# Performance work log

Hardware: AMD Instinct MI355X
Metric: run time of the kernel (lower is better)

The kernel has to match this reference:

```python
import jax, jax.numpy as jnp
import numpy as np
from jax import lax
import math

D_MODEL, D_STATE, D_CONV, D_INNER, DT_RANK = 1024, 16, 4, 2048, 64
BATCH, SEQLEN = 2, 2048


def setup_inputs() -> dict:
    key = jax.random.key(0)
    ks = jax.random.split(key, 10)
    s = 0.02
    x = jax.random.normal(ks[0], (BATCH, SEQLEN, D_MODEL), jnp.float32)
    W_in = jax.random.normal(ks[1], (D_MODEL, 2 * D_INNER), jnp.float32) * s
    conv_w = jax.random.normal(ks[2], (D_INNER, 1, D_CONV), jnp.float32) * 0.2
    conv_b = jnp.zeros((D_INNER,), jnp.float32)
    W_x = jax.random.normal(ks[3], (D_INNER, DT_RANK + 2 * D_STATE), jnp.float32) * s
    W_dt = jax.random.normal(ks[4], (DT_RANK, D_INNER), jnp.float32) * s
    # dt bias init as in the torch module: inverse-softplus of dt ~ logU(1e-3, 1e-1)
    u = jax.random.uniform(ks[5], (D_INNER,), jnp.float32)
    dt = jnp.clip(jnp.exp(u * (math.log(0.1) - math.log(0.001)) + math.log(0.001)), 1e-4)
    b_dt = dt + jnp.log(-jnp.expm1(-dt))
    A_log = jnp.log(jnp.tile(jnp.arange(1, D_STATE + 1, dtype=jnp.float32)[None, :], (D_INNER, 1)))
    D = jnp.ones((D_INNER,), jnp.float32)
    W_out = jax.random.normal(ks[6], (D_INNER, D_MODEL), jnp.float32) * s
    return {"x": x, "W_in": W_in, "conv_w": conv_w, "conv_b": conv_b, "W_x": W_x,
            "W_dt": W_dt, "b_dt": b_dt, "A_log": A_log, "D": D, "W_out": W_out}


def _forward(x, W_in, conv_w, conv_b, W_x, W_dt, b_dt, A_log, D, W_out):
    b, l, _ = x.shape
    d_inner, d_state = A_log.shape
    d_conv = conv_w.shape[-1]
    dt_rank = W_dt.shape[0]

    xz = x @ W_in                                  # (b, l, 2*d_inner)
    xi, z = jnp.split(xz, 2, axis=-1)

    # depthwise causal conv1d (torch pads both sides by d_conv-1 then slices [:l])
    xc = jnp.transpose(xi, (0, 2, 1))              # (b, d_inner, l)
    xc = lax.conv_general_dilated(
        xc, conv_w, window_strides=(1,), padding=[(d_conv - 1, 0)],
        feature_group_count=d_inner,
        dimension_numbers=("NCH", "OIH", "NCH"))
    xc = xc + conv_b[None, :, None]
    xi = jax.nn.silu(jnp.transpose(xc, (0, 2, 1)))  # (b, l, d_inner)

    x_dbl = xi @ W_x                                # (b, l, dt_rank + 2*d_state)
    dt, B, C = jnp.split(x_dbl, [dt_rank, dt_rank + d_state], axis=-1)
    dt = jax.nn.softplus(dt @ W_dt + b_dt)          # (b, l, d_inner)
    A = -jnp.exp(A_log)                             # (d_inner, d_state)

    def step(h, inp):
        dt_t, B_t, C_t, x_t = inp                   # (b,d),(b,n),(b,n),(b,d)
        dA = jnp.exp(dt_t[..., None] * A)           # (b, d, n)
        dB = dt_t[..., None] * B_t[:, None, :]      # (b, d, n)
        h = dA * h + dB * x_t[..., None]
        y = jnp.einsum("bdn,bn->bd", h, C_t) + D * x_t
        return h, y

    xs = (jnp.transpose(dt, (1, 0, 2)), jnp.transpose(B, (1, 0, 2)),
          jnp.transpose(C, (1, 0, 2)), jnp.transpose(xi, (1, 0, 2)))
    h0 = jnp.zeros((b, d_inner, d_state), x.dtype)
    _, ys = lax.scan(step, h0, xs)                  # ys: (l, b, d_inner)
    y = jnp.transpose(ys, (1, 0, 2))

    y = y * jax.nn.silu(z)
    return y @ W_out                                # (b, l, d_model)


def reference(x, W_in, conv_w, conv_b, W_x, W_dt, b_dt, A_log, D, W_out):
    return _forward(x, W_in, conv_w, conv_b, W_x, W_dt, b_dt, A_log, D, W_out)
```

## Files before the change

### kernel.cpp

```cpp
#include <hip/hip_runtime.h>
#include <math.h>


#define D_INNER 2048
#define D_STATE 16
#define SEQLEN  2048
#define NBATCH  2
#define NCHUNK  32
#define CHUNKLEN (SEQLEN / NCHUNK)

using f32x4 = __attribute__((ext_vector_type(4))) float;
using s16x8 = __attribute__((ext_vector_type(8))) short;

__device__ __forceinline__ float siluf(float x) {
  return x / (1.f + __expf(-x));
}
__device__ __forceinline__ float softplusf(float x) {
  return fmaxf(x, 0.f) + log1pf(__expf(-fabsf(x)));
}

__device__ __forceinline__ void split_pair(float f0, float f1,
                                           unsigned& hw, unsigned& lw) {
  unsigned b0 = __float_as_uint(f0), b1 = __float_as_uint(f1);
  hw = (b0 >> 16) | (b1 & 0xFFFF0000u);
  float r0 = f0 - __uint_as_float(b0 & 0xFFFF0000u);
  float r1 = f1 - __uint_as_float(b1 & 0xFFFF0000u);
  unsigned c0 = __float_as_uint(r0); c0 += 0x7FFFu + ((c0 >> 16) & 1u);
  unsigned c1 = __float_as_uint(r1); c1 += 0x7FFFu + ((c1 >> 16) & 1u);
  lw = (c0 >> 16) | (c1 & 0xFFFF0000u);
}

__global__ __launch_bounds__(256) void packsplit_k(
    const float* __restrict__ in, unsigned* __restrict__ out)
{
  size_t g = (size_t)blockIdx.x * 256 + threadIdx.x;
  float f[32];
#pragma unroll
  for (int q = 0; q < 8; ++q)
    *(float4*)&f[q * 4] = *(const float4*)(in + g * 32 + q * 4);
  unsigned* o = out + g * 32;
#pragma unroll
  for (int j = 0; j < 16; ++j) {
    unsigned hw, lw;
    split_pair(f[2 * j], f[2 * j + 1], hw, lw);
    o[j] = hw; o[16 + j] = lw;
  }
}

__global__ __launch_bounds__(256) void packsplit_dt_k(
    const float* __restrict__ xdbl, unsigned* __restrict__ out)
{
  int g = blockIdx.x * 256 + threadIdx.x;
  int row = g >> 1, kc = g & 1;
  float f[32];
#pragma unroll
  for (int q = 0; q < 8; ++q)
    *(float4*)&f[q * 4] =
        *(const float4*)(xdbl + (size_t)row * 96 + kc * 32 + q * 4);
  unsigned* o = out + (size_t)g * 32;
#pragma unroll
  for (int j = 0; j < 16; ++j) {
    unsigned hw, lw;
    split_pair(f[2 * j], f[2 * j + 1], hw, lw);
    o[j] = hw; o[16 + j] = lw;
  }
}

__global__ __launch_bounds__(256) void transpack_k(
    const float* __restrict__ in, unsigned* __restrict__ out, int K, int N)
{
  __shared__ float tile[32][257];
  const int tid = threadIdx.x;
  const int nb = blockIdx.x * 256;
  const int kc = blockIdx.y;
#pragma unroll 8
  for (int ky = 0; ky < 32; ++ky)
    tile[ky][tid] = in[(size_t)(kc * 32 + ky) * N + nb + tid];
  __syncthreads();
  unsigned* o = out + ((size_t)(nb + tid) * (K >> 5) + kc) * 32;
#pragma unroll
  for (int j = 0; j < 16; ++j) {
    unsigned hw, lw;
    split_pair(tile[2 * j][tid], tile[2 * j + 1][tid], hw, lw);
    o[j] = hw; o[16 + j] = lw;
  }
}

__global__ __launch_bounds__(128) void transpack_wx_k(
    const float* __restrict__ Wx, unsigned* __restrict__ out)
{
  const int n = threadIdx.x;
  const int kc = blockIdx.x;
  float f[32];
#pragma unroll
  for (int j = 0; j < 32; ++j)
    f[j] = (n < 96) ? Wx[(size_t)(kc * 32 + j) * 96 + n] : 0.f;
  unsigned* o = out + ((size_t)n * 64 + kc) * 32;
#pragma unroll
  for (int j = 0; j < 16; ++j) {
    unsigned hw, lw;
    split_pair(f[2 * j], f[2 * j + 1], hw, lw);
    o[j] = hw; o[16 + j] = lw;
  }
}

template <int EPI>
__global__ __launch_bounds__(256, 2) void mgemm_split(
    const unsigned short* __restrict__ A, const unsigned short* __restrict__ Bt,
    const float* __restrict__ bias, float* __restrict__ C,
    int M, int N, int K, int ldc)
{
  __shared__ s16x8 AsV[128 * 8];
  __shared__ s16x8 BsV[128 * 8];

  const int tid = threadIdx.x;
  const int wv  = tid >> 6;
  const int ln  = tid & 63;
  const int wr  = wv >> 1, wc = wv & 1;
  const int m0  = blockIdx.y * 128, n0 = blockIdx.x * 128;
  const int K32 = K >> 5;

  const int rr = ln & 15;
  const int ko = ln >> 4;
  const int sh = ko ^ (rr & 7);
  const int sl = (4 | ko) ^ (rr & 7);
  const int srow  = ln >> 3;
  const int sslot = (ln & 7) ^ srow;

  f32x4 acc[4][4];
#pragma unroll
  for (int i = 0; i < 4; i++)
#pragma unroll
    for (int j = 0; j < 4; j++) acc[i][j] = (f32x4)0.f;

  for (int ktc = 0; ktc < K32; ++ktc) {
    __syncthreads();
#pragma unroll
    for (int t = 0; t < 4; ++t) {
      int i = wv * 4 + t;
      const unsigned short* ga =
          A + ((size_t)(m0 + i * 8 + srow) * K32 + ktc) * 64 + sslot * 8;
      const unsigned short* gb =
          Bt + ((size_t)(n0 + i * 8 + srow) * K32 + ktc) * 64 + sslot * 8;
      __builtin_amdgcn_global_load_lds(
          (const __attribute__((address_space(1))) void*)ga,
          (__attribute__((address_space(3))) void*)((char*)AsV + i * 1024), 16, 0, 0);
      __builtin_amdgcn_global_load_lds(
          (const __attribute__((address_space(1))) void*)gb,
          (__attribute__((address_space(3))) void*)((char*)BsV + i * 1024), 16, 0, 0);
    }
    __syncthreads();

    s16x8 ah[4], al[4], bh[4], bl[4];
#pragma unroll
    for (int mi = 0; mi < 4; ++mi) {
      int r = wr * 64 + mi * 16 + rr;
      ah[mi] = AsV[r * 8 + sh];
      al[mi] = AsV[r * 8 + sl];
    }
#pragma unroll
    for (int ni = 0; ni < 4; ++ni) {
      int c = wc * 64 + ni * 16 + rr;
      bh[ni] = BsV[c * 8 + sh];
      bl[ni] = BsV[c * 8 + sl];
    }
#pragma unroll
    for (int mi = 0; mi < 4; ++mi)
#pragma unroll
      for (int ni = 0; ni < 4; ++ni) {
        acc[mi][ni] = __builtin_amdgcn_mfma_f32_16x16x32_bf16(ah[mi], bh[ni], acc[mi][ni], 0, 0, 0);
        acc[mi][ni] = __builtin_amdgcn_mfma_f32_16x16x32_bf16(ah[mi], bl[ni], acc[mi][ni], 0, 0, 0);
        acc[mi][ni] = __builtin_amdgcn_mfma_f32_16x16x32_bf16(al[mi], bh[ni], acc[mi][ni], 0, 0, 0);
      }
  }

  const int orow = (ln >> 4) * 4;
#pragma unroll
  for (int mi = 0; mi < 4; ++mi)
#pragma unroll
    for (int ni = 0; ni < 4; ++ni) {
      int rowg = m0 + wr * 64 + mi * 16 + orow;
      int colg = n0 + wc * 64 + ni * 16 + rr;
      float bcol = (EPI == 1) ? bias[colg] : 0.f;
#pragma unroll
      for (int i = 0; i < 4; ++i) {
        float v = acc[mi][ni][i];
        if (EPI == 1) v = softplusf(v + bcol);
        C[(size_t)(rowg + i) * ldc + colg] = v;
      }
    }
}

__global__ __launch_bounds__(256, 2) void xdbl_mfma_k(
    const unsigned short* __restrict__ A, const unsigned short* __restrict__ Bt,
    float* __restrict__ P)
{
  __shared__ s16x8 AsV[128 * 8];
  __shared__ s16x8 BsV[128 * 8];

  const int tid = threadIdx.x;
  const int wv  = tid >> 6;
  const int ln  = tid & 63;
  const int wr  = wv >> 1, wc = wv & 1;
  const int kz  = blockIdx.x;
  const int m0  = blockIdx.y * 128;
  const int K32 = 64;

  const int rr = ln & 15;
  const int ko = ln >> 4;
  const int sh = ko ^ (rr & 7);
  const int sl = (4 | ko) ^ (rr & 7);
  const int srow  = ln >> 3;
  const int sslot = (ln & 7) ^ srow;

  f32x4 acc[4][4];
#pragma unroll
  for (int i = 0; i < 4; i++)
#pragma unroll
    for (int j = 0; j < 4; j++) acc[i][j] = (f32x4)0.f;

  for (int ktc = kz * 8; ktc < kz * 8 + 8; ++ktc) {
    __syncthreads();
#pragma unroll
    for (int t = 0; t < 4; ++t) {
      int i = wv * 4 + t;
      const unsigned short* ga =
          A + ((size_t)(m0 + i * 8 + srow) * K32 + ktc) * 64 + sslot * 8;
      const unsigned short* gb =
          Bt + ((size_t)(i * 8 + srow) * K32 + ktc) * 64 + sslot * 8;
      __builtin_amdgcn_global_load_lds(
          (const __attribute__((address_space(1))) void*)ga,
          (__attribute__((address_space(3))) void*)((char*)AsV + i * 1024), 16, 0, 0);
      __builtin_amdgcn_global_load_lds(
          (const __attribute__((address_space(1))) void*)gb,
          (__attribute__((address_space(3))) void*)((char*)BsV + i * 1024), 16, 0, 0);
    }
    __syncthreads();

    s16x8 ah[4], al[4], bh[4], bl[4];
#pragma unroll
    for (int mi = 0; mi < 4; ++mi) {
      int r = wr * 64 + mi * 16 + rr;
      ah[mi] = AsV[r * 8 + sh];
      al[mi] = AsV[r * 8 + sl];
    }
#pragma unroll
    for (int ni = 0; ni < 4; ++ni) {
      int c = wc * 64 + ni * 16 + rr;
      bh[ni] = BsV[c * 8 + sh];
      bl[ni] = BsV[c * 8 + sl];
    }
#pragma unroll
    for (int mi = 0; mi < 4; ++mi)
#pragma unroll
      for (int ni = 0; ni < 4; ++ni) {
        acc[mi][ni] = __builtin_amdgcn_mfma_f32_16x16x32_bf16(ah[mi], bh[ni], acc[mi][ni], 0, 0, 0);
        acc[mi][ni] = __builtin_amdgcn_mfma_f32_16x16x32_bf16(ah[mi], bl[ni], acc[mi][ni], 0, 0, 0);
        acc[mi][ni] = __builtin_amdgcn_mfma_f32_16x16x32_bf16(al[mi], bh[ni], acc[mi][ni], 0, 0, 0);
      }
  }

  const int orow = (ln >> 4) * 4;
#pragma unroll
  for (int mi = 0; mi < 4; ++mi)
#pragma unroll
    for (int ni = 0; ni < 4; ++ni) {
      int rowg = m0 + wr * 64 + mi * 16 + orow;
      int colg = wc * 64 + ni * 16 + rr;
      if (colg < 96) {
#pragma unroll
        for (int i = 0; i < 4; ++i)
          P[((size_t)kz * 4096 + rowg + i) * 96 + colg] = acc[mi][ni][i];
      }
    }
}

__global__ __launch_bounds__(256) void xdbl_reduce_k(
    const float* __restrict__ P, float* __restrict__ xdbl)
{
  int i = blockIdx.x * 256 + threadIdx.x;
  float s = 0.f;
#pragma unroll
  for (int kz = 0; kz < 8; ++kz) s += P[(size_t)kz * 393216 + i];
  xdbl[i] = s;
}

__global__ __launch_bounds__(256) void conv_silu_k(
    const float* __restrict__ xz, const float* __restrict__ cw,
    const float* __restrict__ cb, float* __restrict__ xi)
{
  int idx = blockIdx.x * 256 + threadIdx.x;
  int d = idx & (D_INNER - 1);
  int row = idx >> 11;
  int l = row & (SEQLEN - 1);
  float4 w = *(const float4*)(cw + d * 4);
  const float wv[4] = {w.x, w.y, w.z, w.w};
  float acc = cb[d];
#pragma unroll
  for (int j = 0; j < 4; j++) {
    int ll = l - 3 + j;
    if (ll >= 0)
      acc = fmaf(wv[j], xz[(size_t)(row - 3 + j) * 4096 + d], acc);
  }
  xi[idx] = siluf(acc);
}

__global__ __launch_bounds__(256) void aprep_k(const float* __restrict__ A_log,
                                               float* __restrict__ A2)
{
  int i = blockIdx.x * 256 + threadIdx.x;
  A2[i] = -__expf(A_log[i]);
}

__global__ __launch_bounds__(256) void scan_pass1(
    const float* __restrict__ dt, const float* __restrict__ xi,
    const float* __restrict__ xdbl, const float* __restrict__ A2,
    float* __restrict__ cP, float* __restrict__ cH)
{
  int d = blockIdx.x * 256 + threadIdx.x;
  int c = blockIdx.y;
  int b = blockIdx.z;
  float a2[D_STATE], h[D_STATE], P[D_STATE];
#pragma unroll
  for (int n = 0; n < D_STATE; n++) {
    a2[n] = A2[d * D_STATE + n];
    h[n] = 0.f;
    P[n] = 1.f;
  }
  int rowbase = b * SEQLEN + c * CHUNKLEN;
  for (int l = 0; l < CHUNKLEN; l++) {
    int row = rowbase + l;
    float dtv = dt[(size_t)row * D_INNER + d];
    float xv = xi[(size_t)row * D_INNER + d];
    float dtx = dtv * xv;
    const float* Bp = xdbl + (size_t)row * 96 + 64;
#pragma unroll
    for (int n = 0; n < D_STATE; n++) {
      float dA = __expf(dtv * a2[n]);
      P[n] *= dA;
      h[n] = fmaf(dA, h[n], dtx * Bp[n]);
    }
  }
  size_t base = ((size_t)(b * D_INNER + d) * NCHUNK + c) * D_STATE;
#pragma unroll
  for (int n = 0; n < D_STATE; n++) {
    cP[base + n] = P[n];
    cH[base + n] = h[n];
  }
}

__global__ __launch_bounds__(256) void scan_pass2(
    const float* __restrict__ cP, float* __restrict__ cH)
{
  int t = blockIdx.x * 256 + threadIdx.x;
  size_t base = (size_t)(t >> 4) * (NCHUNK * D_STATE) + (t & 15);
  float h = 0.f;
  for (int c = 0; c < NCHUNK; c++) {
    size_t idx = base + (size_t)c * D_STATE;
    float Pv = cP[idx];
    float q = cH[idx];
    cH[idx] = h;
    h = fmaf(Pv, h, q);
  }
}

__global__ __launch_bounds__(256) void scan_pass3(
    float* __restrict__ dtyg, const float* __restrict__ xi,
    const float* __restrict__ xdbl, const float* __restrict__ A2,
    const float* __restrict__ cH, const float* __restrict__ Dvec,
    const float* __restrict__ xz)
{
  int d = blockIdx.x * 256 + threadIdx.x;
  int c = blockIdx.y;
  int b = blockIdx.z;
  float a2[D_STATE], h[D_STATE];
  size_t base = ((size_t)(b * D_INNER + d) * NCHUNK + c) * D_STATE;
#pragma unroll
  for (int n = 0; n < D_STATE; n++) {
    a2[n] = A2[d * D_STATE + n];
    h[n] = cH[base + n];
  }
  float Dd = Dvec[d];
  int rowbase = b * SEQLEN + c * CHUNKLEN;
  for (int l = 0; l < CHUNKLEN; l++) {
    int row = rowbase + l;
    float dtv = dtyg[(size_t)row * D_INNER + d];
    float xv = xi[(size_t)row * D_INNER + d];
    float dtx = dtv * xv;
    const float* Bp = xdbl + (size_t)row * 96 + 64;
    const float* Cp = Bp + D_STATE;
    float y = Dd * xv;
#pragma unroll
    for (int n = 0; n < D_STATE; n++) {
      float dA = __expf(dtv * a2[n]);
      h[n] = fmaf(dA, h[n], dtx * Bp[n]);
      y = fmaf(h[n], Cp[n], y);
    }
    float z = xz[(size_t)row * 4096 + D_INNER + d];
    dtyg[(size_t)row * D_INNER + d] = y * siluf(z);
  }
}

extern "C" void kernel_launch(void* const* d_in, const int* in_sizes, int n_in,
                              void* d_out, int out_size, void* d_ws,
                              size_t ws_size, hipStream_t stream)
{
  const float* x     = (const float*)d_in[0];
  const float* W_in  = (const float*)d_in[1];
  const float* cw    = (const float*)d_in[2];
  const float* cb    = (const float*)d_in[3];
  const float* W_x   = (const float*)d_in[4];
  const float* W_dt  = (const float*)d_in[5];
  const float* b_dt  = (const float*)d_in[6];
  const float* A_log = (const float*)d_in[7];
  const float* Dv    = (const float*)d_in[8];
  const float* W_out = (const float*)d_in[9];
  float* out = (float*)d_out;

  float* ws    = (float*)d_ws;
  float* xz    = ws;
  float* xi    = xz + 16777216;
  float* xdbl  = xi + 8388608;
  float* dtyg  = xdbl + 393216;
  float* A2    = dtyg + 8388608;
  float* cP    = A2 + 32768;
  float* cH    = cP + 2097152;

  unsigned* WinTP  = (unsigned*)dtyg;
  unsigned* xP     = (unsigned*)(dtyg + 4194304);
  unsigned* xiP    = (unsigned*)dtyg;
  unsigned* WxTP   = (unsigned*)xdbl;
  float*    Ppart  = cP;
  unsigned* xdblP  = (unsigned*)cP;
  unsigned* WdtTP  = (unsigned*)cP + 262144;
  unsigned* ygP    = (unsigned*)xi;
  unsigned* WoutTP = (unsigned*)cP;

  aprep_k<<<128, 256, 0, stream>>>(A_log, A2);

  transpack_k<<<dim3(16, 32), 256, 0, stream>>>(W_in, WinTP, 1024, 4096);
  packsplit_k<<<512, 256, 0, stream>>>(x, xP);

  mgemm_split<0><<<dim3(32, 32), 256, 0, stream>>>(
      (const unsigned short*)xP, (const unsigned short*)WinTP, nullptr, xz,
      4096, 4096, 1024, 4096);

  conv_silu_k<<<32768, 256, 0, stream>>>(xz, cw, cb, xi);

  packsplit_k<<<1024, 256, 0, stream>>>(xi, xiP);
  transpack_wx_k<<<64, 128, 0, stream>>>(W_x, WxTP);
  xdbl_mfma_k<<<dim3(8, 32), 256, 0, stream>>>(
      (const unsigned short*)xiP, (const unsigned short*)WxTP, Ppart);
  xdbl_reduce_k<<<1536, 256, 0, stream>>>(Ppart, xdbl);

  packsplit_dt_k<<<32, 256, 0, stream>>>(xdbl, xdblP);
  transpack_k<<<dim3(8, 2), 256, 0, stream>>>(W_dt, WdtTP, 64, 2048);
  mgemm_split<1><<<dim3(16, 32), 256, 0, stream>>>(
      (const unsigned short*)xdblP, (const unsigned short*)WdtTP, b_dt, dtyg,
      4096, 2048, 64, 2048);

  scan_pass1<<<dim3(8, NCHUNK, NBATCH), 256, 0, stream>>>(dtyg, xi, xdbl, A2, cP, cH);
  scan_pass2<<<256, 256, 0, stream>>>(cP, cH);
  scan_pass3<<<dim3(8, NCHUNK, NBATCH), 256, 0, stream>>>(dtyg, xi, xdbl, A2, cH, Dv, xz);

  packsplit_k<<<1024, 256, 0, stream>>>(dtyg, ygP);
  transpack_k<<<dim3(4, 64), 256, 0, stream>>>(W_out, WoutTP, 2048, 1024);

  mgemm_split<0><<<dim3(8, 32), 256, 0, stream>>>(
      (const unsigned short*)ygP, (const unsigned short*)WoutTP, nullptr, out,
      4096, 1024, 2048, 1024);
}
```

Baseline: 486.6 us.

## Fuse hi/lo bf16 split packing into producer kernels and drop A prep kernel

```diff
diff --git a/kernel.cpp b/kernel.cpp
--- a/kernel.cpp
+++ b/kernel.cpp
@@ -30,6 +30,16 @@
   lw = (c0 >> 16) | (c1 & 0xFFFF0000u);
 }
 
+__device__ __forceinline__ void split_one(float v, unsigned short& hv,
+                                          unsigned short& lv) {
+  unsigned b = __float_as_uint(v);
+  hv = (unsigned short)(b >> 16);
+  float r = v - __uint_as_float(b & 0xFFFF0000u);
+  unsigned c = __float_as_uint(r);
+  c += 0x7FFFu + ((c >> 16) & 1u);
+  lv = (unsigned short)(c >> 16);
+}
+
 __global__ __launch_bounds__(256) void packsplit_k(
     const float* __restrict__ in, unsigned* __restrict__ out)
 {
@@ -39,25 +49,6 @@
   for (int q = 0; q < 8; ++q)
     *(float4*)&f[q * 4] = *(const float4*)(in + g * 32 + q * 4);
   unsigned* o = out + g * 32;
-#pragma unroll
-  for (int j = 0; j < 16; ++j) {
-    unsigned hw, lw;
-    split_pair(f[2 * j], f[2 * j + 1], hw, lw);
-    o[j] = hw; o[16 + j] = lw;
-  }
-}
-
-__global__ __launch_bounds__(256) void packsplit_dt_k(
-    const float* __restrict__ xdbl, unsigned* __restrict__ out)
-{
-  int g = blockIdx.x * 256 + threadIdx.x;
-  int row = g >> 1, kc = g & 1;
-  float f[32];
-#pragma unroll
-  for (int q = 0; q < 8; ++q)
-    *(float4*)&f[q * 4] =
-        *(const float4*)(xdbl + (size_t)row * 96 + kc * 32 + q * 4);
-  unsigned* o = out + (size_t)g * 32;
 #pragma unroll
   for (int j = 0; j < 16; ++j) {
     unsigned hw, lw;
@@ -108,7 +99,7 @@
 __global__ __launch_bounds__(256, 2) void mgemm_split(
     const unsigned short* __restrict__ A, const unsigned short* __restrict__ Bt,
     const float* __restrict__ bias, float* __restrict__ C,
-    int M, int N, int K, int ldc)
+    int M, int N, int K, int ldaC, int ldc)
 {
   __shared__ s16x8 AsV[128 * 8];
   __shared__ s16x8 BsV[128 * 8];
@@ -139,7 +130,7 @@
     for (int t = 0; t < 4; ++t) {
       int i = wv * 4 + t;
       const unsigned short* ga =
-          A + ((size_t)(m0 + i * 8 + srow) * K32 + ktc) * 64 + sslot * 8;
+          A + ((size_t)(m0 + i * 8 + srow) * ldaC + ktc) * 64 + sslot * 8;
       const unsigned short* gb =
           Bt + ((size_t)(n0 + i * 8 + srow) * K32 + ktc) * 64 + sslot * 8;
       __builtin_amdgcn_global_load_lds(
@@ -275,19 +266,31 @@
     }
 }
 
-__global__ __launch_bounds__(256) void xdbl_reduce_k(
-    const float* __restrict__ P, float* __restrict__ xdbl)
+__global__ __launch_bounds__(256) void xdbl_fuse_k(
+    const float* __restrict__ P, float* __restrict__ xdbl,
+    unsigned short* __restrict__ xdblPs)
 {
   int i = blockIdx.x * 256 + threadIdx.x;
   float s = 0.f;
 #pragma unroll
   for (int kz = 0; kz < 8; ++kz) s += P[(size_t)kz * 393216 + i];
-  xdbl[i] = s;
-}
-
-__global__ __launch_bounds__(256) void conv_silu_k(
+  int row = i / 96;
+  int col = i - row * 96;
+  if (col < 64) {
+    unsigned short hv, lv;
+    split_one(s, hv, lv);
+    size_t cb = ((size_t)row * 2 + (col >> 5)) * 64 + (col & 31);
+    xdblPs[cb] = hv;
+    xdblPs[cb + 32] = lv;
+  } else {
+    xdbl[i] = s;
+  }
+}
+
+__global__ __launch_bounds__(256) void conv_silu_pack_k(
     const float* __restrict__ xz, const float* __restrict__ cw,
-    const float* __restrict__ cb, float* __restrict__ xi)
+    const float* __restrict__ cb, float* __restrict__ xi,
+    unsigned short* __restrict__ xiPs)
 {
   int idx = blockIdx.x * 256 + threadIdx.x;
   int d = idx & (D_INNER - 1);
@@ -302,19 +305,18 @@
     if (ll >= 0)
       acc = fmaf(wv[j], xz[(size_t)(row - 3 + j) * 4096 + d], acc);
   }
-  xi[idx] = siluf(acc);
-}
-
-__global__ __launch_bounds__(256) void aprep_k(const float* __restrict__ A_log,
-                                               float* __restrict__ A2)
-{
-  int i = blockIdx.x * 256 + threadIdx.x;
-  A2[i] = -__expf(A_log[i]);
+  float v = siluf(acc);
+  xi[idx] = v;
+  unsigned short hv, lv;
+  split_one(v, hv, lv);
+  size_t cbase = ((size_t)row * 64 + (d >> 5)) * 64 + (d & 31);
+  xiPs[cbase] = hv;
+  xiPs[cbase + 32] = lv;
 }
 
 __global__ __launch_bounds__(256) void scan_pass1(
     const float* __restrict__ dt, const float* __restrict__ xi,
-    const float* __restrict__ xdbl, const float* __restrict__ A2,
+    const float* __restrict__ xdbl, const float* __restrict__ A_log,
     float* __restrict__ cP, float* __restrict__ cH)
 {
   int d = blockIdx.x * 256 + threadIdx.x;
@@ -323,7 +325,7 @@
   float a2[D_STATE], h[D_STATE], P[D_STATE];
 #pragma unroll
   for (int n = 0; n < D_STATE; n++) {
-    a2[n] = A2[d * D_STATE + n];
+    a2[n] = -__expf(A_log[d * D_STATE + n]);
     h[n] = 0.f;
     P[n] = 1.f;
   }
@@ -365,10 +367,10 @@
 }
 
 __global__ __launch_bounds__(256) void scan_pass3(
-    float* __restrict__ dtyg, const float* __restrict__ xi,
-    const float* __restrict__ xdbl, const float* __restrict__ A2,
+    const float* __restrict__ dt, const float* __restrict__ xi,
+    const float* __restrict__ xdbl, const float* __restrict__ A_log,
     const float* __restrict__ cH, const float* __restrict__ Dvec,
-    const float* __restrict__ xz)
+    float* __restrict__ xz)
 {
   int d = blockIdx.x * 256 + threadIdx.x;
   int c = blockIdx.y;
@@ -377,14 +379,15 @@
   size_t base = ((size_t)(b * D_INNER + d) * NCHUNK + c) * D_STATE;
 #pragma unroll
   for (int n = 0; n < D_STATE; n++) {
-    a2[n] = A2[d * D_STATE + n];
+    a2[n] = -__expf(A_log[d * D_STATE + n]);
     h[n] = cH[base + n];
   }
   float Dd = Dvec[d];
+  unsigned short* ygPs = (unsigned short*)xz;
   int rowbase = b * SEQLEN + c * CHUNKLEN;
   for (int l = 0; l < CHUNKLEN; l++) {
     int row = rowbase + l;
-    float dtv = dtyg[(size_t)row * D_INNER + d];
+    float dtv = dt[(size_t)row * D_INNER + d];
     float xv = xi[(size_t)row * D_INNER + d];
     float dtx = dtv * xv;
     const float* Bp = xdbl + (size_t)row * 96 + 64;
@@ -397,7 +400,12 @@
       y = fmaf(h[n], Cp[n], y);
     }
     float z = xz[(size_t)row * 4096 + D_INNER + d];
-    dtyg[(size_t)row * D_INNER + d] = y * siluf(z);
+    float g = y * siluf(z);
+    unsigned short hv, lv;
+    split_one(g, hv, lv);
+    size_t cb = (size_t)row * 8192 + (size_t)(d >> 5) * 64 + (d & 31);
+    ygPs[cb] = hv;
+    ygPs[cb + 32] = lv;
   }
 }
 
@@ -425,48 +433,44 @@
   float* A2    = dtyg + 8388608;
   float* cP    = A2 + 32768;
   float* cH    = cP + 2097152;
+  (void)A2;
 
   unsigned* WinTP  = (unsigned*)dtyg;
   unsigned* xP     = (unsigned*)(dtyg + 4194304);
   unsigned* xiP    = (unsigned*)dtyg;
   unsigned* WxTP   = (unsigned*)xdbl;
   float*    Ppart  = cP;
-  unsigned* xdblP  = (unsigned*)cP;
-  unsigned* WdtTP  = (unsigned*)cP + 262144;
-  unsigned* ygP    = (unsigned*)xi;
+  unsigned short* xdblPs = (unsigned short*)(cP + 3145728);
+  unsigned* WdtTP  = (unsigned*)(cP + 3145728 + 262144);
+  unsigned short* ygPs   = (unsigned short*)xz;
   unsigned* WoutTP = (unsigned*)cP;
-
-  aprep_k<<<128, 256, 0, stream>>>(A_log, A2);
 
   transpack_k<<<dim3(16, 32), 256, 0, stream>>>(W_in, WinTP, 1024, 4096);
   packsplit_k<<<512, 256, 0, stream>>>(x, xP);
 
   mgemm_split<0><<<dim3(32, 32), 256, 0, stream>>>(
       (const unsigned short*)xP, (const unsigned short*)WinTP, nullptr, xz,
-      4096, 4096, 1024, 4096);
-
-  conv_silu_k<<<32768, 256, 0, stream>>>(xz, cw, cb, xi);
-
-  packsplit_k<<<1024, 256, 0, stream>>>(xi, xiP);
+      4096, 4096, 1024, 32, 4096);
+
+  conv_silu_pack_k<<<32768, 256, 0, stream>>>(xz, cw, cb, xi, (unsigned short*)xiP);
+
   transpack_wx_k<<<64, 128, 0, stream>>>(W_x, WxTP);
   xdbl_mfma_k<<<dim3(8, 32), 256, 0, stream>>>(
       (const unsigned short*)xiP, (const unsigned short*)WxTP, Ppart);
-  xdbl_reduce_k<<<1536, 256, 0, stream>>>(Ppart, xdbl);
-
-  packsplit_dt_k<<<32, 256, 0, stream>>>(xdbl, xdblP);
+  xdbl_fuse_k<<<1536, 256, 0, stream>>>(Ppart, xdbl, xdblPs);
+
   transpack_k<<<dim3(8, 2), 256, 0, stream>>>(W_dt, WdtTP, 64, 2048);
   mgemm_split<1><<<dim3(16, 32), 256, 0, stream>>>(
-      (const unsigned short*)xdblP, (const unsigned short*)WdtTP, b_dt, dtyg,
-      4096, 2048, 64, 2048);
-
-  scan_pass1<<<dim3(8, NCHUNK, NBATCH), 256, 0, stream>>>(dtyg, xi, xdbl, A2, cP, cH);
+      xdblPs, (const unsigned short*)WdtTP, b_dt, dtyg,
+      4096, 2048, 64, 2, 2048);
+
+  scan_pass1<<<dim3(8, NCHUNK, NBATCH), 256, 0, stream>>>(dtyg, xi, xdbl, A_log, cP, cH);
   scan_pass2<<<256, 256, 0, stream>>>(cP, cH);
-  scan_pass3<<<dim3(8, NCHUNK, NBATCH), 256, 0, stream>>>(dtyg, xi, xdbl, A2, cH, Dv, xz);
-
-  packsplit_k<<<1024, 256, 0, stream>>>(dtyg, ygP);
+  scan_pass3<<<dim3(8, NCHUNK, NBATCH), 256, 0, stream>>>(dtyg, xi, xdbl, A_log, cH, Dv, xz);
+
   transpack_k<<<dim3(4, 64), 256, 0, stream>>>(W_out, WoutTP, 2048, 1024);
 
   mgemm_split<0><<<dim3(8, 32), 256, 0, stream>>>(
-      (const unsigned short*)ygP, (const unsigned short*)WoutTP, nullptr, out,
-      4096, 1024, 2048, 1024);
-}
+      ygPs, (const unsigned short*)WoutTP, nullptr, out,
+      4096, 1024, 2048, 128, 1024);
+}
```

New measurement: 450.7 us. 1.08x faster.
